# Performance work log

Measured on AMD Instinct MI355X. Metric: run time of the kernel, lower is better.

Reference implementation:

```python
import jax, jax.numpy as jnp
import numpy as np

N, E, G = 20000, 160000, 32          # nodes, edges, graphs in batch
F_IN, H, P, C = 67, 2048, 1024, 18   # in_feat, hidden_feat, fc2 width, n_classifier
EPS = 1e-5
SLOPE = 0.01  # leaky_relu default negative slope


def setup_inputs() -> dict:
    key = jax.random.key(0)
    ks = jax.random.split(key, 24)
    w = lambda k, shape: (jax.random.normal(k, shape, jnp.float32) * 0.02)
    return {
        "h": jax.random.normal(ks[0], (N, F_IN), jnp.float32),
        "src": jax.random.randint(ks[1], (E,), 0, N),
        "dst": jax.random.randint(ks[2], (E,), 0, N),
        "gids": jnp.sort(jax.random.randint(ks[3], (N,), 0, G)),
        # SAGEConv layers: fc_self, fc_neigh (no per-fc bias), shared bias
        "ws1": w(ks[4], (F_IN, H)), "wn1": w(ks[5], (F_IN, H)), "b1": jnp.zeros((H,), jnp.float32),
        "ws2": w(ks[6], (H, H)),    "wn2": w(ks[7], (H, H)),    "b2": jnp.zeros((H,), jnp.float32),
        "ws3": w(ks[8], (H, H)),    "wn3": w(ks[9], (H, H)),    "b3": jnp.zeros((H,), jnp.float32),
        # batch norms (gamma, beta)
        "g1": jnp.ones((H,), jnp.float32), "be1": jnp.zeros((H,), jnp.float32),
        "g2": jnp.ones((H,), jnp.float32), "be2": jnp.zeros((H,), jnp.float32),
        "g3": jnp.ones((H,), jnp.float32), "be3": jnp.zeros((H,), jnp.float32),
        # MLP head
        "fw1": w(ks[10], (H, H)), "fb1": jnp.zeros((H,), jnp.float32),
        "fw2": w(ks[11], (H, P)), "fb2": jnp.zeros((P,), jnp.float32),
        "fw3": w(ks[12], (P, C)), "fb3": jnp.zeros((C,), jnp.float32),
    }


def _leaky(x):
    return jnp.where(x >= 0, x, SLOPE * x)


def _sage(x, src, dst, w_self, w_neigh, b):
    # DGL SAGEConv 'mean': mean of neighbor (src) features into dst, then linears.
    nsum = jax.ops.segment_sum(x[src], dst, num_segments=N)            # [N, F]
    deg = jax.ops.segment_sum(jnp.ones((E,), x.dtype), dst, num_segments=N)
    neigh = nsum / jnp.maximum(deg, 1.0)[:, None]                      # 0 for isolated
    return x @ w_self + neigh @ w_neigh + b


def _bn(x, gamma, beta):
    m = x.mean(0)
    v = x.var(0)
    return (x - m) * jax.lax.rsqrt(v + EPS) * gamma + beta


def reference(h, src, dst, gids,
              ws1, wn1, b1, g1, be1,
              ws2, wn2, b2, g2, be2,
              ws3, wn3, b3, g3, be3,
              fw1, fb1, fw2, fb2, fw3, fb3):
    x = _leaky(_bn(_sage(h, src, dst, ws1, wn1, b1), g1, be1))
    x = _leaky(_bn(_sage(x, src, dst, ws2, wn2, b2), g2, be2))
    x = _leaky(_bn(_sage(x, src, dst, ws3, wn3, b3), g3, be3))
    # mean pooling per graph
    gsum = jax.ops.segment_sum(x, gids, num_segments=G)                # [G, H]
    cnt = jax.ops.segment_sum(jnp.ones((N,), x.dtype), gids, num_segments=G)
    hg = gsum / jnp.maximum(cnt, 1.0)[:, None]
    # dropouts are identity in eval
    y = _leaky(hg @ fw1 + fb1)
    y = _leaky(y @ fw2 + fb2)
    return y @ fw3 + fb3
```

## Files before the change

### kernel.cpp

```cpp
#include <hip/hip_runtime.h>

typedef unsigned short u16;
typedef __attribute__((ext_vector_type(4))) float f32x4;
typedef __attribute__((ext_vector_type(8))) __bf16 bf16x8;
typedef __attribute__((ext_vector_type(8))) short s16x8;
typedef __attribute__((ext_vector_type(4))) u16 u16x4;

#define N_NODES 20000
#define N_EDGES 160000
#define N_GRAPH 32
#define F_IN 67
#define HID 2048
#define PW 1024
#define NCLS 18
#define MPAD 20096
#define MPAD2 20224
#define K1 192

__device__ __forceinline__ float bf2f(u16 u) {
    unsigned v = ((unsigned)u) << 16;
    float f; __builtin_memcpy(&f, &v, 4); return f;
}
__device__ __forceinline__ u16 f2bf(float f) {
    unsigned u; __builtin_memcpy(&u, &f, 4);
    u = (u + 0x7FFF + ((u >> 16) & 1)) >> 16;
    return (u16)u;
}
__device__ __forceinline__ int imax(int a, int b) { return a > b ? a : b; }

__device__ __forceinline__ void ld16(const u16* gptr, u16* lptr) {
    __builtin_amdgcn_global_load_lds(
        (const __attribute__((address_space(1))) unsigned int*)gptr,
        (__attribute__((address_space(3))) unsigned int*)lptr,
        16, 0, 0);
}

__global__ void k_hist(const int* __restrict__ dst, int* __restrict__ cnt) {
    int e = blockIdx.x * 256 + threadIdx.x;
    if (e < N_EDGES) atomicAdd(&cnt[dst[e]], 1);
}

__global__ void k_scan(const int* __restrict__ cnt, int* __restrict__ rowptr) {
    __shared__ int part[256];
    int t = threadIdx.x;
    const int per = (N_NODES + 255) / 256;
    int base = t * per;
    int s = 0;
    for (int i = 0; i < per; i++) { int idx = base + i; if (idx < N_NODES) s += cnt[idx]; }
    part[t] = s; __syncthreads();
    for (int off = 1; off < 256; off <<= 1) {
        int v = (t >= off) ? part[t - off] : 0;
        __syncthreads();
        part[t] += v;
        __syncthreads();
    }
    int running = (t == 0) ? 0 : part[t - 1];
    for (int i = 0; i < per; i++) {
        int idx = base + i;
        if (idx < N_NODES) { rowptr[idx] = running; running += cnt[idx]; }
    }
    if (t == 255) rowptr[N_NODES] = running;
}

__global__ void k_scatter(const int* __restrict__ src, const int* __restrict__ dst,
                          const int* __restrict__ rowptr, int* __restrict__ cursor,
                          int* __restrict__ csr) {
    int e = blockIdx.x * 256 + threadIdx.x;
    if (e < N_EDGES) {
        int d = dst[e];
        int p = atomicAdd(&cursor[d], 1);
        csr[rowptr[d] + p] = src[e];
    }
}

__global__ void k_w1t(const float* __restrict__ ws1, const float* __restrict__ wn1,
                      u16* __restrict__ w1t) {
    int n = blockIdx.x, t = threadIdx.x;
    float v = 0.f;
    if (t < F_IN) v = ws1[(size_t)t * HID + n];
    else if (t < 2 * F_IN) v = wn1[(size_t)(t - F_IN) * HID + n];
    w1t[(size_t)n * K1 + t] = f2bf(v);
}

__global__ void k_transpose(const float* __restrict__ src, u16* __restrict__ dst, int colofs) {
    __shared__ float tile[32][33];
    int bx = blockIdx.x * 32, by = blockIdx.y * 32;
    int tx = threadIdx.x, ty = threadIdx.y;
#pragma unroll
    for (int i = 0; i < 32; i += 8)
        tile[ty + i][tx] = src[(size_t)(by + ty + i) * HID + bx + tx];
    __syncthreads();
#pragma unroll
    for (int i = 0; i < 32; i += 8)
        dst[(size_t)(bx + ty + i) * (2 * HID) + colofs + by + tx] = f2bf(tile[tx][ty + i]);
}

__global__ void k_agg1(const float* __restrict__ h, const int* __restrict__ rowptr,
                       const int* __restrict__ csr, u16* __restrict__ acat) {
    int n = blockIdx.x, t = threadIdx.x;
    if (t < F_IN) {
        acat[(size_t)n * K1 + t] = f2bf(h[(size_t)n * F_IN + t]);
    } else if (t < 2 * F_IN) {
        int c = t - F_IN;
        int e0 = rowptr[n], e1 = rowptr[n + 1];
        float a = 0.f;
        for (int e = e0; e < e1; e++) a += h[(size_t)csr[e] * F_IN + c];
        acat[(size_t)n * K1 + F_IN + c] = f2bf(a / (float)imax(e1 - e0, 1));
    }
}

__global__ __launch_bounds__(256)
void k_agg(const u16* __restrict__ x, const int* __restrict__ rowptr,
           const int* __restrict__ csr, u16* __restrict__ out) {
    int n = blockIdx.x, t = threadIdx.x;
    int e0 = rowptr[n], e1 = rowptr[n + 1];
    float acc[8] = {0, 0, 0, 0, 0, 0, 0, 0};
    for (int e = e0; e < e1; e++) {
        int s = csr[e];
        s16x8 v = *(const s16x8*)&x[(size_t)s * HID + t * 8];
#pragma unroll
        for (int j = 0; j < 8; j++) acc[j] += bf2f((u16)v[j]);
    }
    float inv = 1.0f / (float)imax(e1 - e0, 1);
    s16x8 o;
#pragma unroll
    for (int j = 0; j < 8; j++) o[j] = (short)f2bf(acc[j] * inv);
    *(s16x8*)&out[(size_t)n * HID + t * 8] = o;
}

__global__ __launch_bounds__(256)
void k_gemm(const u16* __restrict__ A0, const u16* __restrict__ A1, int ksplit,
            const u16* __restrict__ WT, u16* __restrict__ C,
            int ldA, int K, int ldC) {
    __shared__ u16 As[128 * 64];
    __shared__ u16 Bs[128 * 64];
    const int tid = threadIdx.x;
    const int lane = tid & 63;
    const int wave = tid >> 6;
    const int wr = (wave >> 1) * 64;
    const int wc = (wave & 1) * 64;
    const int lr = lane & 15;
    const int lk = (lane >> 4) * 8;
    const size_t row0 = (size_t)blockIdx.x * 128;
    const int col0 = blockIdx.y * 128;

    f32x4 acc[4][4];
#pragma unroll
    for (int i = 0; i < 4; i++)
#pragma unroll
        for (int j = 0; j < 4; j++) acc[i][j] = f32x4{0.f, 0.f, 0.f, 0.f};

    int rr[4], cc[4], lo[4];
#pragma unroll
    for (int i = 0; i < 4; i++) {
        int chunk = i * 256 + tid;
        rr[i] = chunk >> 3;
        cc[i] = (chunk & 7) * 8;
        lo[i] = (i * 256 + (wave << 6)) * 8;
    }
    size_t abase[4], bbase[4];
#pragma unroll
    for (int i = 0; i < 4; i++) {
        abase[i] = (row0 + rr[i]) * (size_t)ldA + cc[i];
        bbase[i] = ((size_t)col0 + rr[i]) * (size_t)K + cc[i];
    }

    for (int kt = 0; kt < K; kt += 64) {
        const u16* Asrc; int kc;
        if (kt < ksplit) { Asrc = A0; kc = kt; } else { Asrc = A1; kc = kt - ksplit; }
#pragma unroll
        for (int i = 0; i < 4; i++) {
            ld16(Asrc + abase[i] + kc, &As[lo[i]]);
            ld16(WT + bbase[i] + kt, &Bs[lo[i]]);
        }
        __syncthreads();
#pragma unroll
        for (int kk = 0; kk < 2; kk++) {
            bf16x8 af[4], bw[4];
#pragma unroll
            for (int i = 0; i < 4; i++)
                af[i] = *(const bf16x8*)&As[(wr + i * 16 + lr) * 64 + kk * 32 + lk];
#pragma unroll
            for (int j = 0; j < 4; j++)
                bw[j] = *(const bf16x8*)&Bs[(wc + j * 16 + lr) * 64 + kk * 32 + lk];
#pragma unroll
            for (int i = 0; i < 4; i++)
#pragma unroll
                for (int j = 0; j < 4; j++)
                    acc[i][j] = __builtin_amdgcn_mfma_f32_16x16x32_bf16(bw[j], af[i], acc[i][j], 0, 0, 0);
        }
        __syncthreads();
    }
#pragma unroll
    for (int i = 0; i < 4; i++) {
        size_t m = row0 + wr + i * 16 + lr;
#pragma unroll
        for (int j = 0; j < 4; j++) {
            int nb = col0 + wc + j * 16 + (lane >> 4) * 4;
            u16x4 o;
#pragma unroll
            for (int rg = 0; rg < 4; rg++) o[rg] = f2bf(acc[i][j][rg]);
            *(u16x4*)&C[m * (size_t)ldC + nb] = o;
        }
    }
}

#define VM4 asm volatile("s_waitcnt vmcnt(4)" ::: "memory")
#define VM2 asm volatile("s_waitcnt vmcnt(2)" ::: "memory")
#define VM0 asm volatile("s_waitcnt vmcnt(0)" ::: "memory")
#define VMNONE asm volatile("" ::: "memory")

#define STAGE_A(H) { const u16* as_ = (kt1 < 32 ? A0 : A1);                        \
    size_t ko_ = (size_t)(kt1 & 31) * 64 + swe;                                     \
    ld16(as_ + (row0 + 0 * 128 + (H) * 64 + r8) * 2048 + ko_,                       \
         LA + dbo + ((H) * 128 + 0 * 64 + r8) * 64 + ld8);                          \
    ld16(as_ + (row0 + 1 * 128 + (H) * 64 + r8) * 2048 + ko_,                       \
         LA + dbo + ((H) * 128 + 1 * 64 + r8) * 64 + ld8); }

#define STAGE_B(H) { size_t ko_ = (size_t)kt1 * 64 + swe;                           \
    ld16(WT + ((size_t)col0 + ((r8 >> 5)) * 64 + (H) * 32 + (r8 & 31)) * 4096 + ko_,\
         LB + dbo + ((H) * 128 + 0 * 64 + r8) * 64 + ld8);                          \
    ld16(WT + ((size_t)col0 + (2 + (r8 >> 5)) * 64 + (H) * 32 + (r8 & 31)) * 4096 + ko_,\
         LB + dbo + ((H) * 128 + 1 * 64 + r8) * 64 + ld8); }

#define PHASE(QM, QN, STG, WAIT) {                                                  \
    bf16x8 af[4][2], bw[2][2];                                                      \
    _Pragma("unroll") for (int f = 0; f < 4; ++f)                                   \
      _Pragma("unroll") for (int kk = 0; kk < 2; ++kk)                              \
        af[f][kk] = *(const bf16x8*)(bA + (QM) * 16384 + (wm * 64 + f * 16 + lr) * 128 \
                                     + ((kk * 64 + lg * 16) ^ rxor));               \
    _Pragma("unroll") for (int n = 0; n < 2; ++n)                                   \
      _Pragma("unroll") for (int kk = 0; kk < 2; ++kk)                              \
        bw[n][kk] = *(const bf16x8*)(bB + (QN) * 16384 + (wn * 32 + n * 16 + lr) * 128 \
                                     + ((kk * 64 + lg * 16) ^ rxor));               \
    STG;                                                                            \
    WAIT;                                                                           \
    __builtin_amdgcn_s_barrier();                                                   \
    asm volatile("s_waitcnt lgkmcnt(0)" ::: "memory");                              \
    __builtin_amdgcn_sched_barrier(0);                                              \
    __builtin_amdgcn_s_setprio(1);                                                  \
    _Pragma("unroll") for (int kk = 0; kk < 2; ++kk)                                \
      _Pragma("unroll") for (int f = 0; f < 4; ++f)                                 \
        _Pragma("unroll") for (int n = 0; n < 2; ++n)                               \
          acc[(QM) * 4 + f][(QN) * 2 + n] = __builtin_amdgcn_mfma_f32_16x16x32_bf16(\
              bw[n][kk], af[f][kk], acc[(QM) * 4 + f][(QN) * 2 + n], 0, 0, 0);      \
    __builtin_amdgcn_s_setprio(0); }

__global__ __launch_bounds__(512, 2)
void k_gemm256(const u16* __restrict__ A0, const u16* __restrict__ A1,
               const u16* __restrict__ WT, u16* __restrict__ C) {
    __shared__ u16 LA[2 * 256 * 64];
    __shared__ u16 LB[2 * 256 * 64];
    const int tid = threadIdx.x;
    const int lane = tid & 63;
    const int wave = tid >> 6;
    const int wm = wave >> 2, wn = wave & 3;
    const int lr = lane & 15, lg = lane >> 4;
    const int rxor = (lr & 7) << 4;

    const int f2 = (blockIdx.x & 7) * 79 + (blockIdx.x >> 3);
    const size_t row0 = (size_t)(f2 % 79) * 256;
    const int col0 = (f2 / 79) * 256;

    const int r8 = tid >> 3;
    const int ld8 = (tid & 7) * 8;
    const int swe = ((ld8 * 2) ^ ((r8 & 7) << 4)) >> 1;

    f32x4 acc[8][4];
#pragma unroll
    for (int i = 0; i < 8; i++)
#pragma unroll
        for (int j = 0; j < 4; j++) acc[i][j] = f32x4{0.f, 0.f, 0.f, 0.f};

    {
        const int kt1 = 0; const int dbo = 0;
        STAGE_A(0) STAGE_B(0) STAGE_A(1) STAGE_B(1)
    }
    VM4;
    __builtin_amdgcn_s_barrier();

    for (int t = 0; t < 63; ++t) {
        const char* bA = (const char*)LA + (t & 1) * 32768;
        const char* bB = (const char*)LB + (t & 1) * 32768;
        const int kt1 = t + 1;
        const int dbo = ((t & 1) ^ 1) * 16384;
        PHASE(0, 0, STAGE_A(0), VM4)
        PHASE(1, 0, STAGE_B(0), VM4)
        PHASE(0, 1, STAGE_A(1), VMNONE)
        PHASE(1, 1, STAGE_B(1), VM4)
    }
    {
        const char* bA = (const char*)LA + 32768;
        const char* bB = (const char*)LB + 32768;
        PHASE(0, 0, {}, VM2)
        PHASE(1, 0, {}, VM0)
        PHASE(0, 1, {}, VMNONE)
        PHASE(1, 1, {}, VMNONE)
    }

#pragma unroll
    for (int f = 0; f < 8; ++f) {
        size_t m = row0 + wm * 128 + f * 16 + lr;
#pragma unroll
        for (int n = 0; n < 4; ++n) {
            int cb = col0 + wn * 64 + n * 16 + lg * 4;
            u16x4 o;
#pragma unroll
            for (int rg = 0; rg < 4; ++rg) o[rg] = f2bf(acc[f][n][rg]);
            *(u16x4*)&C[m * HID + cb] = o;
        }
    }
}

__global__ __launch_bounds__(256)
void k_stats(const u16* __restrict__ x, float* __restrict__ ssum, float* __restrict__ ssq) {
    int t = threadIdx.x;
    int r0 = blockIdx.x * 100;
    float s[8] = {}, s2[8] = {};
    for (int i = 0; i < 100; ++i) {
        s16x8 v = *(const s16x8*)&x[(size_t)(r0 + i) * HID + t * 8];
#pragma unroll
        for (int j = 0; j < 8; ++j) { float f = bf2f((u16)v[j]); s[j] += f; s2[j] += f * f; }
    }
#pragma unroll
    for (int j = 0; j < 8; ++j) {
        atomicAdd(&ssum[t * 8 + j], s[j]);
        atomicAdd(&ssq[t * 8 + j], s2[j]);
    }
}

__global__ void k_bnfin(const float* __restrict__ ssum, const float* __restrict__ ssq,
                        const float* __restrict__ gma, const float* __restrict__ bta,
                        float* __restrict__ aco, float* __restrict__ dco) {
    int c = blockIdx.x * 256 + threadIdx.x;
    float m = ssum[c] * (1.0f / N_NODES);
    float v = ssq[c] * (1.0f / N_NODES) - m * m;
    float a = gma[c] * rsqrtf(v + 1e-5f);
    aco[c] = a;
    dco[c] = bta[c] - m * a;
}

__global__ void k_bnleaky(const u16* __restrict__ xin, const float* __restrict__ aco,
                          const float* __restrict__ dco, u16* __restrict__ xout) {
    size_t eb = ((size_t)blockIdx.x * 256 + threadIdx.x) * 8;
    int col = (int)(eb & (HID - 1));
    s16x8 v = *(const s16x8*)&xin[eb];
    s16x8 o;
#pragma unroll
    for (int j = 0; j < 8; j++) {
        float f = bf2f((u16)v[j]) * aco[col + j] + dco[col + j];
        f = f > 0.f ? f : 0.01f * f;
        o[j] = (short)f2bf(f);
    }
    *(s16x8*)&xout[eb] = o;
}

__global__ void k_bounds(const int* __restrict__ gids, int* __restrict__ gstart) {
    int t = threadIdx.x;
    if (t > N_GRAPH) return;
    int lo = 0, hi = N_NODES;
    while (lo < hi) { int mid = (lo + hi) >> 1; if (gids[mid] < t) lo = mid + 1; else hi = mid; }
    gstart[t] = lo;
}

__global__ void k_pool(const u16* __restrict__ x, const int* __restrict__ gstart,
                       float* __restrict__ hg) {
    int g = blockIdx.x;
    int col = blockIdx.y * 256 + threadIdx.x;
    int r0 = gstart[g], r1 = gstart[g + 1];
    float s = 0.f;
    for (int r = r0; r < r1; r++) s += bf2f(x[(size_t)r * HID + col]);
    hg[(size_t)g * HID + col] = s / (float)imax(r1 - r0, 1);
}

__global__ __launch_bounds__(256)
void k_mlp_part(const float* __restrict__ X, const float* __restrict__ W,
                float* __restrict__ Yp, int K, int Nc) {
    __shared__ float xs[32 * 256];
    int t = threadIdx.x;
    int kc = blockIdx.y;
    int n = blockIdx.x * 64 + (t & 63);
    int mg = t >> 6;
#pragma unroll
    for (int l = 0; l < 32; ++l) {
        int e = l * 256 + t;
        xs[e] = X[(size_t)(e >> 8) * K + kc * 256 + (e & 255)];
    }
    __syncthreads();
    float acc[8] = {};
    for (int k = 0; k < 256; ++k) {
        float wv = W[(size_t)(kc * 256 + k) * Nc + n];
#pragma unroll
        for (int i = 0; i < 8; ++i) acc[i] += xs[(mg * 8 + i) * 256 + k] * wv;
    }
#pragma unroll
    for (int i = 0; i < 8; ++i)
        Yp[(size_t)(kc * 32 + mg * 8 + i) * Nc + n] = acc[i];
}

__global__ void k_mlp_red(const float* __restrict__ Yp, const float* __restrict__ bias,
                          float* __restrict__ Y, int Nc, int leaky) {
    int idx = blockIdx.x * 256 + threadIdx.x;
    int n = idx % Nc;
    float s = 0.f;
#pragma unroll
    for (int kc = 0; kc < 8; ++kc) s += Yp[(size_t)kc * 32 * Nc + idx];
    float v = s + bias[n];
    if (leaky) v = v > 0.f ? v : 0.01f * v;
    Y[idx] = v;
}

__global__ void k_fc3(const float* __restrict__ y2, const float* __restrict__ fw3,
                      const float* __restrict__ fb3, float* __restrict__ out) {
    __shared__ float red[8][32];
    int m = blockIdx.x, t = threadIdx.x;
    int ch = t >> 5, c = t & 31;
    float s = 0.f;
    if (c < NCLS) {
        for (int j = 0; j < 128; ++j) {
            int k = ch * 128 + j;
            s += y2[(size_t)m * PW + k] * fw3[(size_t)k * NCLS + c];
        }
    }
    red[ch][c] = s;
    __syncthreads();
    if (t < NCLS) {
        float a = 0.f;
#pragma unroll
        for (int c2 = 0; c2 < 8; ++c2) a += red[c2][t];
        out[m * NCLS + t] = a + fb3[t];
    }
}

extern "C" void kernel_launch(void* const* d_in, const int* in_sizes, int n_in,
                              void* d_out, int out_size, void* d_ws, size_t ws_size,
                              hipStream_t stream) {
    const float* h   = (const float*)d_in[0];
    const int* src   = (const int*)d_in[1];
    const int* dst   = (const int*)d_in[2];
    const int* gids  = (const int*)d_in[3];
    const float* ws1 = (const float*)d_in[4];
    const float* wn1 = (const float*)d_in[5];
    const float* ws2 = (const float*)d_in[7];
    const float* wn2 = (const float*)d_in[8];
    const float* ws3 = (const float*)d_in[10];
    const float* wn3 = (const float*)d_in[11];
    const float* g1  = (const float*)d_in[13];
    const float* be1 = (const float*)d_in[14];
    const float* g2  = (const float*)d_in[15];
    const float* be2 = (const float*)d_in[16];
    const float* g3  = (const float*)d_in[17];
    const float* be3 = (const float*)d_in[18];
    const float* fw1 = (const float*)d_in[19];
    const float* fb1 = (const float*)d_in[20];
    const float* fw2 = (const float*)d_in[21];
    const float* fb2 = (const float*)d_in[22];
    const float* fw3 = (const float*)d_in[23];
    const float* fb3 = (const float*)d_in[24];
    float* out = (float*)d_out;
    (void)in_sizes; (void)n_in; (void)out_size;

    char* base = (char*)d_ws;
    size_t off = 0;
    auto alloc = [&](size_t b) -> char* {
        char* p = base + off;
        off += (b + 255) & ~(size_t)255;
        return p;
    };
    u16* BUF0 = (u16*)alloc((size_t)MPAD2 * HID * 2);
    u16* BUF1 = (u16*)alloc((size_t)MPAD2 * HID * 2);
    u16* BUF2 = (u16*)alloc((size_t)MPAD2 * HID * 2);
    u16* WT   = (u16*)alloc((size_t)HID * 2 * HID * 2);
    int* cnt    = (int*)alloc(N_NODES * 4);
    int* rowptr = (int*)alloc((N_NODES + 1) * 4);
    int* cursor = (int*)alloc(N_NODES * 4);
    int* csr    = (int*)alloc(N_EDGES * 4);
    float* ssum = (float*)alloc(HID * 4);
    float* ssq  = (float*)alloc(HID * 4);
    float* aco  = (float*)alloc(HID * 4);
    float* dco  = (float*)alloc(HID * 4);
    int* gstart = (int*)alloc(64 * 4);
    float* hg = (float*)alloc((size_t)N_GRAPH * HID * 4);
    float* y1 = (float*)alloc((size_t)N_GRAPH * HID * 4);
    float* y2 = (float*)alloc((size_t)N_GRAPH * PW * 4);
    u16* ACAT = (u16*)((char*)BUF2);
    u16* W1T  = (u16*)((char*)BUF2 + (size_t)MPAD * K1 * 2);
    float* Yp = (float*)((char*)BUF2);

    if (off > ws_size) return;

    hipMemsetAsync(cnt, 0, N_NODES * 4, stream);
    hipMemsetAsync(cursor, 0, N_NODES * 4, stream);
    hipMemsetAsync(ACAT, 0, (size_t)MPAD * K1 * 2, stream);

    k_hist<<<(N_EDGES + 255) / 256, 256, 0, stream>>>(dst, cnt);
    k_scan<<<1, 256, 0, stream>>>(cnt, rowptr);
    k_scatter<<<(N_EDGES + 255) / 256, 256, 0, stream>>>(src, dst, rowptr, cursor, csr);

    k_w1t<<<HID, K1, 0, stream>>>(ws1, wn1, W1T);
    k_agg1<<<N_NODES, 192, 0, stream>>>(h, rowptr, csr, ACAT);

    dim3 gg(MPAD / 128, HID / 128);
    dim3 tb(32, 8);
    k_gemm<<<gg, 256, 0, stream>>>(ACAT, ACAT, K1, W1T, BUF0, K1, K1, HID);
    hipMemsetAsync(ssum, 0, 2 * HID * 4, stream);
    k_stats<<<200, 256, 0, stream>>>(BUF0, ssum, ssq);
    k_bnfin<<<HID / 256, 256, 0, stream>>>(ssum, ssq, g1, be1, aco, dco);
    k_bnleaky<<<20000, 256, 0, stream>>>(BUF0, aco, dco, BUF1);
    k_transpose<<<dim3(64, 64), tb, 0, stream>>>(ws2, WT, 0);
    k_transpose<<<dim3(64, 64), tb, 0, stream>>>(wn2, WT, HID);
    k_agg<<<N_NODES, 256, 0, stream>>>(BUF1, rowptr, csr, BUF2);
    k_gemm256<<<632, 512, 0, stream>>>(BUF1, BUF2, WT, BUF0);
    hipMemsetAsync(ssum, 0, 2 * HID * 4, stream);
    k_stats<<<200, 256, 0, stream>>>(BUF0, ssum, ssq);
    k_bnfin<<<HID / 256, 256, 0, stream>>>(ssum, ssq, g2, be2, aco, dco);
    k_bnleaky<<<20000, 256, 0, stream>>>(BUF0, aco, dco, BUF1);
    k_transpose<<<dim3(64, 64), tb, 0, stream>>>(ws3, WT, 0);
    k_transpose<<<dim3(64, 64), tb, 0, stream>>>(wn3, WT, HID);
    k_agg<<<N_NODES, 256, 0, stream>>>(BUF1, rowptr, csr, BUF2);
    k_gemm256<<<632, 512, 0, stream>>>(BUF1, BUF2, WT, BUF0);
    hipMemsetAsync(ssum, 0, 2 * HID * 4, stream);
    k_stats<<<200, 256, 0, stream>>>(BUF0, ssum, ssq);
    k_bnfin<<<HID / 256, 256, 0, stream>>>(ssum, ssq, g3, be3, aco, dco);
    k_bnleaky<<<20000, 256, 0, stream>>>(BUF0, aco, dco, BUF1);
    k_bounds<<<1, 64, 0, stream>>>(gids, gstart);
    k_pool<<<dim3(N_GRAPH, HID / 256), 256, 0, stream>>>(BUF1, gstart, hg);
    k_mlp_part<<<dim3(HID / 64, 8), 256, 0, stream>>>(hg, fw1, Yp, HID, HID);
    k_mlp_red<<<(N_GRAPH * HID) / 256, 256, 0, stream>>>(Yp, fb1, y1, HID, 1);
    k_mlp_part<<<dim3(PW / 64, 8), 256, 0, stream>>>(y1, fw2, Yp, HID, PW);
    k_mlp_red<<<(N_GRAPH * PW) / 256, 256, 0, stream>>>(Yp, fb2, y2, PW, 1);
    k_fc3<<<N_GRAPH, 256, 0, stream>>>(y2, fw3, fb3, out);
}
```

Before: 1.620 ms.

## Replace four-phase interleaved GEMM pipeline with single-stage prefetch per K tile

After: 1.693 ms. 4.5% more time.

```diff
diff --git a/kernel.cpp b/kernel.cpp
--- a/kernel.cpp
+++ b/kernel.cpp
@@ -205,11 +205,6 @@
     }
 }
 
-#define VM4 asm volatile("s_waitcnt vmcnt(4)" ::: "memory")
-#define VM2 asm volatile("s_waitcnt vmcnt(2)" ::: "memory")
-#define VM0 asm volatile("s_waitcnt vmcnt(0)" ::: "memory")
-#define VMNONE asm volatile("" ::: "memory")
-
 #define STAGE_A(H) { const u16* as_ = (kt1 < 32 ? A0 : A1);                        \
     size_t ko_ = (size_t)(kt1 & 31) * 64 + swe;                                     \
     ld16(as_ + (row0 + 0 * 128 + (H) * 64 + r8) * 2048 + ko_,                       \
@@ -222,29 +217,6 @@
          LB + dbo + ((H) * 128 + 0 * 64 + r8) * 64 + ld8);                          \
     ld16(WT + ((size_t)col0 + (2 + (r8 >> 5)) * 64 + (H) * 32 + (r8 & 31)) * 4096 + ko_,\
          LB + dbo + ((H) * 128 + 1 * 64 + r8) * 64 + ld8); }
-
-#define PHASE(QM, QN, STG, WAIT) {                                                  \
-    bf16x8 af[4][2], bw[2][2];                                                      \
-    _Pragma("unroll") for (int f = 0; f < 4; ++f)                                   \
-      _Pragma("unroll") for (int kk = 0; kk < 2; ++kk)                              \
-        af[f][kk] = *(const bf16x8*)(bA + (QM) * 16384 + (wm * 64 + f * 16 + lr) * 128 \
-                                     + ((kk * 64 + lg * 16) ^ rxor));               \
-    _Pragma("unroll") for (int n = 0; n < 2; ++n)                                   \
-      _Pragma("unroll") for (int kk = 0; kk < 2; ++kk)                              \
-        bw[n][kk] = *(const bf16x8*)(bB + (QN) * 16384 + (wn * 32 + n * 16 + lr) * 128 \
-                                     + ((kk * 64 + lg * 16) ^ rxor));               \
-    STG;                                                                            \
-    WAIT;                                                                           \
-    __builtin_amdgcn_s_barrier();                                                   \
-    asm volatile("s_waitcnt lgkmcnt(0)" ::: "memory");                              \
-    __builtin_amdgcn_sched_barrier(0);                                              \
-    __builtin_amdgcn_s_setprio(1);                                                  \
-    _Pragma("unroll") for (int kk = 0; kk < 2; ++kk)                                \
-      _Pragma("unroll") for (int f = 0; f < 4; ++f)                                 \
-        _Pragma("unroll") for (int n = 0; n < 2; ++n)                               \
-          acc[(QM) * 4 + f][(QN) * 2 + n] = __builtin_amdgcn_mfma_f32_16x16x32_bf16(\
-              bw[n][kk], af[f][kk], acc[(QM) * 4 + f][(QN) * 2 + n], 0, 0, 0);      \
-    __builtin_amdgcn_s_setprio(0); }
 
 __global__ __launch_bounds__(512, 2)
 void k_gemm256(const u16* __restrict__ A0, const u16* __restrict__ A1,
@@ -276,26 +248,57 @@
         const int kt1 = 0; const int dbo = 0;
         STAGE_A(0) STAGE_B(0) STAGE_A(1) STAGE_B(1)
     }
-    VM4;
+    asm volatile("s_waitcnt vmcnt(0)" ::: "memory");
     __builtin_amdgcn_s_barrier();
 
-    for (int t = 0; t < 63; ++t) {
+    for (int t = 0; t < 64; ++t) {
         const char* bA = (const char*)LA + (t & 1) * 32768;
         const char* bB = (const char*)LB + (t & 1) * 32768;
-        const int kt1 = t + 1;
-        const int dbo = ((t & 1) ^ 1) * 16384;
-        PHASE(0, 0, STAGE_A(0), VM4)
-        PHASE(1, 0, STAGE_B(0), VM4)
-        PHASE(0, 1, STAGE_A(1), VMNONE)
-        PHASE(1, 1, STAGE_B(1), VM4)
-    }
-    {
-        const char* bA = (const char*)LA + 32768;
-        const char* bB = (const char*)LB + 32768;
-        PHASE(0, 0, {}, VM2)
-        PHASE(1, 0, {}, VM0)
-        PHASE(0, 1, {}, VMNONE)
-        PHASE(1, 1, {}, VMNONE)
+        if (t < 63) {
+            const int kt1 = t + 1;
+            const int dbo = ((t + 1) & 1) * 16384;
+            STAGE_A(0) STAGE_B(0) STAGE_A(1) STAGE_B(1)
+        }
+        __builtin_amdgcn_sched_barrier(0);
+
+        bf16x8 af[2][4][2], bw[2][2][2];
+#pragma unroll
+        for (int qm = 0; qm < 2; ++qm)
+#pragma unroll
+            for (int f = 0; f < 4; ++f)
+#pragma unroll
+                for (int kk = 0; kk < 2; ++kk)
+                    af[qm][f][kk] = *(const bf16x8*)(bA + qm * 16384
+                        + (wm * 64 + qm * 0 + f * 16 + lr) * 128
+                        + ((kk * 64 + lg * 16) ^ rxor));
+#pragma unroll
+        for (int qn = 0; qn < 2; ++qn)
+#pragma unroll
+            for (int n = 0; n < 2; ++n)
+#pragma unroll
+                for (int kk = 0; kk < 2; ++kk)
+                    bw[qn][n][kk] = *(const bf16x8*)(bB + qn * 16384
+                        + (wn * 32 + n * 16 + lr) * 128
+                        + ((kk * 64 + lg * 16) ^ rxor));
+        __builtin_amdgcn_s_setprio(1);
+#pragma unroll
+        for (int kk = 0; kk < 2; ++kk)
+#pragma unroll
+            for (int qm = 0; qm < 2; ++qm)
+#pragma unroll
+                for (int qn = 0; qn < 2; ++qn)
+#pragma unroll
+                    for (int f = 0; f < 4; ++f)
+#pragma unroll
+                        for (int n = 0; n < 2; ++n)
+                            acc[qm * 4 + f][qn * 2 + n] =
+                                __builtin_amdgcn_mfma_f32_16x16x32_bf16(
+                                    bw[qn][n][kk], af[qm][f][kk],
+                                    acc[qm * 4 + f][qn * 2 + n], 0, 0, 0);
+        __builtin_amdgcn_s_setprio(0);
+        asm volatile("s_waitcnt vmcnt(0) lgkmcnt(0)" ::: "memory");
+        __builtin_amdgcn_sched_barrier(0);
+        __builtin_amdgcn_s_barrier();
     }
 
 #pragma unroll
```
